# Kernel tuning notes

Measured on AMD Instinct MI355X. Metric: run time of the kernel, lower is better.

Reference implementation:

```python
import jax, jax.numpy as jnp
import numpy as np

HIDDEN_DIM = 2048
NUM_EXPERTS = 64
TOP_K = 8
NUM_TOKENS = 16384


def setup_inputs() -> dict:
    key = jax.random.key(0)
    k_x, k_w, k_b = jax.random.split(key, 3)
    X = jax.random.normal(k_x, (NUM_TOKENS, HIDDEN_DIM), dtype=jnp.float32)
    # nn.Linear(hidden_dim, num_experts): weight [out, in], bias [out]
    bound = 1.0 / np.sqrt(HIDDEN_DIM)
    W_gate = jax.random.uniform(k_w, (NUM_EXPERTS, HIDDEN_DIM), jnp.float32, -bound, bound)
    b_gate = jax.random.uniform(k_b, (NUM_EXPERTS,), jnp.float32, -bound, bound)
    return {"X": X, "W_gate": W_gate, "b_gate": b_gate}


def reference(X, W_gate, b_gate):
    # gate linear: [T, H] @ [H, E] + [E] -> [T, E]
    router_logits = jnp.einsum('th,eh->te', X, W_gate) + b_gate
    # softmax in float32 (matches dtype=torch.float)
    router_probs = jax.nn.softmax(router_logits.astype(jnp.float32), axis=-1)
    # top-k over experts: [T, K]
    router_weights, selected_experts_indices = jax.lax.top_k(router_probs, TOP_K)
    router_weights = router_weights / jnp.sum(router_weights, axis=-1, keepdims=True)
    router_weights = router_weights.astype(X.dtype)
    # one-hot [T, K, E] -> permute(2,1,0) -> [E, K, T]
    expert_mask = jax.nn.one_hot(selected_experts_indices, NUM_EXPERTS, dtype=jnp.int64 if jax.config.jax_enable_x64 else jnp.int32)
    expert_mask = jnp.transpose(expert_mask, (2, 1, 0))
    return (router_logits, router_weights, selected_experts_indices.astype(jnp.int32), expert_mask)
```

## Files before the change

### kernel.cpp

```cpp
#include <hip/hip_runtime.h>

#define NT 16384
#define NH 2048
#define NE 64
#define TOPK 8

#define TB 32
#define KSTEPS 64
#define KQ 4
#define KSW (KSTEPS / KQ)

#define LOFF 0
#define WOFF (NT * NE)
#define IOFF (WOFF + NT * TOPK)
#define MOFF (IOFF + NT * TOPK)

typedef __attribute__((ext_vector_type(8))) short short8;
typedef __attribute__((ext_vector_type(4))) float floatx4;

union FragU { uint4 u; short8 s; };

__device__ __forceinline__ unsigned pack3(float a, float b, unsigned& w1, unsigned& w2) {
    unsigned au = __float_as_uint(a), bu = __float_as_uint(b);
    unsigned ah0 = au & 0xFFFF0000u, bh0 = bu & 0xFFFF0000u;
    float ra = a - __uint_as_float(ah0);
    float rb = b - __uint_as_float(bh0);
    unsigned ar = __float_as_uint(ra), br = __float_as_uint(rb);
    unsigned ah1 = ar & 0xFFFF0000u, bh1 = br & 0xFFFF0000u;
    float sa = ra - __uint_as_float(ah1);
    float sb = rb - __uint_as_float(bh1);
    w1 = bh1 | (ah1 >> 16);
    w2 = (__float_as_uint(sb) & 0xFFFF0000u) | (__float_as_uint(sa) >> 16);
    return bh0 | (ah0 >> 16);
}

__global__ __launch_bounds__(64)
void wconv_kernel(const float* __restrict__ Wg, uint4* __restrict__ wsp) {
    const int b = blockIdx.x;
    const int t = b >> 2, g = b & 3;
    const int l = threadIdx.x;
    const int e  = g * 16 + (l & 15);
    const int k0 = t * 32 + (l >> 4) * 8;
    const float* src = Wg + (size_t)e * NH + k0;
    float4 w0 = *(const float4*)src;
    float4 w1 = *(const float4*)(src + 4);
    unsigned u1[4], u2[4];
    uint4 p0;
    p0.x = pack3(w0.x, w0.y, u1[0], u2[0]);
    p0.y = pack3(w0.z, w0.w, u1[1], u2[1]);
    p0.z = pack3(w1.x, w1.y, u1[2], u2[2]);
    p0.w = pack3(w1.z, w1.w, u1[3], u2[3]);
    uint4* dst = wsp + (size_t)((t * 4 + g) * 3) * 64 + l;
    dst[0]   = p0;
    dst[64]  = make_uint4(u1[0], u1[1], u1[2], u1[3]);
    dst[128] = make_uint4(u2[0], u2[1], u2[2], u2[3]);
}

__global__ __launch_bounds__(512, 4)
void router_kernel(const float* __restrict__ X, const uint4* __restrict__ wsp,
                   const float* __restrict__ bg, float* __restrict__ out) {
    __shared__ __align__(16) float P[KQ][TB][68];
    __shared__ __align__(16) float Ls[TB][68];

    const int tid = threadIdx.x;
    const int w   = tid >> 6;
    const int kh  = w & 3;
    const int th  = w >> 2;
    const int l   = tid & 63;
    const int lr  = l & 15, lq = l >> 4;
    const int tbase = blockIdx.x * TB;

    floatx4 acc[4];
#pragma unroll
    for (int g = 0; g < 4; g++) acc[g] = (floatx4)0.0f;

    const float* xp0 = X + (size_t)(tbase + th * 16 + lr) * NH + kh * (KSW * 32) + lq * 8;
    const uint4* wp = wsp + (size_t)(kh * KSW) * 12 * 64 + l;

    float4 a0lo = *(const float4*)xp0;
    float4 a0hi = *(const float4*)(xp0 + 4);

    {
        float4 z = make_float4(0.f, 0.f, 0.f, 0.f);
#pragma unroll
        for (int m = 0; m < 8; m++) {
            int f2  = tid + 512 * m;
            int seg = f2 >> 3;
            int off = (f2 & 7) << 2;
            *(float4*)(out + MOFF + (size_t)seg * NT + tbase + off) = z;
        }
    }

#pragma unroll 2
    for (int t = 0; t < KSW; t++) {
        FragU b[4][3];
        const uint4* wt = wp + t * 768;
#pragma unroll
        for (int g = 0; g < 4; g++)
#pragma unroll
            for (int p = 0; p < 3; p++)
                b[g][p].u = wt[(g * 3 + p) * 64];

        FragU af[3];
        {
            unsigned u1[4], u2[4];
            uint4 q;
            q.x = pack3(a0lo.x, a0lo.y, u1[0], u2[0]);
            q.y = pack3(a0lo.z, a0lo.w, u1[1], u2[1]);
            q.z = pack3(a0hi.x, a0hi.y, u1[2], u2[2]);
            q.w = pack3(a0hi.z, a0hi.w, u1[3], u2[3]);
            af[0].u = q;
            af[1].u = make_uint4(u1[0], u1[1], u1[2], u1[3]);
            af[2].u = make_uint4(u2[0], u2[1], u2[2], u2[3]);
        }

        if (t + 1 < KSW) {
            const float* nx0 = xp0 + (t + 1) * 32;
            a0lo = *(const float4*)nx0;
            a0hi = *(const float4*)(nx0 + 4);
        }

        __builtin_amdgcn_s_setprio(1);
#pragma unroll
        for (int g = 0; g < 4; g++) {
            acc[g] = __builtin_amdgcn_mfma_f32_16x16x32_bf16(af[0].s, b[g][0].s, acc[g], 0, 0, 0);
            acc[g] = __builtin_amdgcn_mfma_f32_16x16x32_bf16(af[0].s, b[g][1].s, acc[g], 0, 0, 0);
            acc[g] = __builtin_amdgcn_mfma_f32_16x16x32_bf16(af[1].s, b[g][0].s, acc[g], 0, 0, 0);
            acc[g] = __builtin_amdgcn_mfma_f32_16x16x32_bf16(af[1].s, b[g][1].s, acc[g], 0, 0, 0);
            acc[g] = __builtin_amdgcn_mfma_f32_16x16x32_bf16(af[0].s, b[g][2].s, acc[g], 0, 0, 0);
            acc[g] = __builtin_amdgcn_mfma_f32_16x16x32_bf16(af[2].s, b[g][0].s, acc[g], 0, 0, 0);
        }
        __builtin_amdgcn_s_setprio(0);
    }

#pragma unroll
    for (int g = 0; g < 4; g++)
#pragma unroll
        for (int r = 0; r < 4; r++)
            P[kh][th * 16 + lq * 4 + r][g * 16 + lr] = acc[g][r];
    __syncthreads();

    {
        int f4  = tid;
        int tok = f4 >> 4;
        int e4  = (f4 & 15) << 2;
        float4 s0 = *(float4*)&P[0][tok][e4];
        float4 s1 = *(float4*)&P[1][tok][e4];
        float4 s2 = *(float4*)&P[2][tok][e4];
        float4 s3 = *(float4*)&P[3][tok][e4];
        float4 bb = *(const float4*)(bg + e4);
        float4 v;
        v.x = s0.x + s1.x + s2.x + s3.x + bb.x;
        v.y = s0.y + s1.y + s2.y + s3.y + bb.y;
        v.z = s0.z + s1.z + s2.z + s3.z + bb.z;
        v.w = s0.w + s1.w + s2.w + s3.w + bb.w;
        *(float4*)&Ls[tok][e4] = v;
        *(float4*)(out + LOFF + (size_t)tbase * NE + (size_t)f4 * 4) = v;
    }
    __syncthreads();

    if (tid < 256) {
        const int tok = tid >> 3;
        const int el  = tid & 7;
        float4 va = *(float4*)&Ls[tok][el * 8];
        float4 vb = *(float4*)&Ls[tok][el * 8 + 4];
        float v[8] = {va.x, va.y, va.z, va.w, vb.x, vb.y, vb.z, vb.w};

        unsigned msk = 0;
        float m0 = 0.f, ssum = 0.f, myv = 0.f;
        int myi = 0;
#pragma unroll
        for (int r = 0; r < 8; r++) {
            float bv = -3.0e38f; int bi = 64;
#pragma unroll
            for (int j = 0; j < 8; j++) {
                bool better = (((msk >> j) & 1u) == 0u) && (v[j] > bv);
                bv = better ? v[j] : bv;
                bi = better ? (el * 8 + j) : bi;
            }
#pragma unroll
            for (int s2 = 1; s2 < 8; s2 <<= 1) {
                float ov = __shfl_xor(bv, s2);
                int   oi = __shfl_xor(bi, s2);
                bool take = (ov > bv) || (ov == bv && oi < bi);
                bv = take ? ov : bv;
                bi = take ? oi : bi;
            }
            if ((bi >> 3) == el) msk |= (1u << (bi & 7));
            if (r == 0) m0 = bv;
            ssum += __expf(bv - m0);
            if (r == el) { myv = bv; myi = bi; }
        }
        float wgt = __expf(myv - m0) / ssum;
        size_t gt = (size_t)(tbase + tok);
        out[WOFF + gt * TOPK + el] = wgt;
        out[IOFF + gt * TOPK + el] = (float)myi;
        out[MOFF + (size_t)myi * (TOPK * NT) + (size_t)el * NT + gt] = 1.0f;
    }
}

extern "C" void kernel_launch(void* const* d_in, const int* in_sizes, int n_in,
                              void* d_out, int out_size, void* d_ws, size_t ws_size,
                              hipStream_t stream) {
    const float* X  = (const float*)d_in[0];
    const float* Wg = (const float*)d_in[1];
    const float* bg = (const float*)d_in[2];
    float* out = (float*)d_out;
    uint4* wsp = (uint4*)d_ws;

    hipLaunchKernelGGL(wconv_kernel, dim3(KSTEPS * 4), dim3(64), 0, stream, Wg, wsp);
    hipLaunchKernelGGL(router_kernel, dim3(NT / TB), dim3(512), 0, stream,
                       X, (const uint4*)wsp, bg, out);
}
```

Baseline: 241.4 us.

## Restage X through LDS with 32x32 MFMA and split top-k into separate kernel

The GEMM now loads X tiles into LDS asynchronously with global_load_lds and double buffering, using an XOR swizzle, and switches from 16x16x32 to 32x32x16 bf16 MFMA with a new weight packing layout. Zeroing of the expert mask moves into the prep kernel. The top-k/softmax stage moves into a third kernel that rereads logits from global memory. The aim is better X load coalescing and MFMA efficiency, at the cost of an extra launch, an extra logits round trip and a per-step barrier.

Result: faster. 224.0 us (-7.2%).

```diff
diff --git a/kernel.cpp b/kernel.cpp
--- a/kernel.cpp
+++ b/kernel.cpp
@@ -6,9 +6,7 @@
 #define TOPK 8
 
 #define TB 32
-#define KSTEPS 64
-#define KQ 4
-#define KSW (KSTEPS / KQ)
+#define NSS 16
 
 #define LOFF 0
 #define WOFF (NT * NE)
@@ -16,9 +14,15 @@
 #define MOFF (IOFF + NT * TOPK)
 
 typedef __attribute__((ext_vector_type(8))) short short8;
-typedef __attribute__((ext_vector_type(4))) float floatx4;
+typedef __attribute__((ext_vector_type(16))) float floatx16;
 
 union FragU { uint4 u; short8 s; };
+
+__device__ __forceinline__ void glds16(const void* g, void* l) {
+    __builtin_amdgcn_global_load_lds(
+        (const __attribute__((address_space(1))) unsigned int*)g,
+        (__attribute__((address_space(3))) unsigned int*)l, 16, 0, 0);
+}
 
 __device__ __forceinline__ unsigned pack3(float a, float b, unsigned& w1, unsigned& w2) {
     unsigned au = __float_as_uint(a), bu = __float_as_uint(b);
@@ -34,169 +38,181 @@
     return bh0 | (ah0 >> 16);
 }
 
-__global__ __launch_bounds__(64)
-void wconv_kernel(const float* __restrict__ Wg, uint4* __restrict__ wsp) {
+__global__ __launch_bounds__(256)
+void prep_kernel(const float* __restrict__ Wg, uint4* __restrict__ wsp,
+                 float* __restrict__ out) {
     const int b = blockIdx.x;
-    const int t = b >> 2, g = b & 3;
-    const int l = threadIdx.x;
-    const int e  = g * 16 + (l & 15);
-    const int k0 = t * 32 + (l >> 4) * 8;
-    const float* src = Wg + (size_t)e * NH + k0;
-    float4 w0 = *(const float4*)src;
-    float4 w1 = *(const float4*)(src + 4);
-    unsigned u1[4], u2[4];
-    uint4 p0;
-    p0.x = pack3(w0.x, w0.y, u1[0], u2[0]);
-    p0.y = pack3(w0.z, w0.w, u1[1], u2[1]);
-    p0.z = pack3(w1.x, w1.y, u1[2], u2[2]);
-    p0.w = pack3(w1.z, w1.w, u1[3], u2[3]);
-    uint4* dst = wsp + (size_t)((t * 4 + g) * 3) * 64 + l;
-    dst[0]   = p0;
-    dst[64]  = make_uint4(u1[0], u1[1], u1[2], u1[3]);
-    dst[128] = make_uint4(u2[0], u2[1], u2[2], u2[3]);
+    const int tid = threadIdx.x;
+
+    float4 z = make_float4(0.f, 0.f, 0.f, 0.f);
+    float4* mp = (float4*)(out + MOFF) + (size_t)b * 8192 + tid;
+#pragma unroll
+    for (int it = 0; it < 32; it++) mp[it * 256] = z;
+
+    if (tid < 64) {
+        const int t = b >> 2, g = (b >> 1) & 1, h = b & 1;
+        const int l = tid;
+        const int e  = g * 32 + (l & 31);
+        const int k0 = t * 32 + h * 16 + (l >> 5) * 8;
+        const float* src = Wg + (size_t)e * NH + k0;
+        float4 w0 = *(const float4*)src;
+        float4 w1 = *(const float4*)(src + 4);
+        unsigned u1[4], u2[4];
+        uint4 p0;
+        p0.x = pack3(w0.x, w0.y, u1[0], u2[0]);
+        p0.y = pack3(w0.z, w0.w, u1[1], u2[1]);
+        p0.z = pack3(w1.x, w1.y, u1[2], u2[2]);
+        p0.w = pack3(w1.z, w1.w, u1[3], u2[3]);
+        const size_t idx0 = (size_t)((t * 2 + g) * 3) * 2 + h;
+        uint4* dst = wsp + idx0 * 64 + l;
+        dst[0]   = p0;
+        dst[128] = make_uint4(u1[0], u1[1], u1[2], u1[3]);
+        dst[256] = make_uint4(u2[0], u2[1], u2[2], u2[3]);
+    }
 }
 
 __global__ __launch_bounds__(512, 4)
-void router_kernel(const float* __restrict__ X, const uint4* __restrict__ wsp,
-                   const float* __restrict__ bg, float* __restrict__ out) {
-    __shared__ __align__(16) float P[KQ][TB][68];
-    __shared__ __align__(16) float Ls[TB][68];
+void gemm_kernel(const float* __restrict__ X, const uint4* __restrict__ wsp,
+                 const float* __restrict__ bg, float* __restrict__ out) {
+    __shared__ float XS[2][4][32][32];
+    __shared__ float P[4][TB][68];
 
     const int tid = threadIdx.x;
-    const int w   = tid >> 6;
-    const int kh  = w & 3;
-    const int th  = w >> 2;
+    const int wv  = tid >> 6;
     const int l   = tid & 63;
-    const int lr  = l & 15, lq = l >> 4;
+    const int eh  = wv & 1;
+    const int kq  = wv >> 1;
+    const int l31 = l & 31;
+    const int lh  = l >> 5;
     const int tbase = blockIdx.x * TB;
 
-    floatx4 acc[4];
-#pragma unroll
-    for (int g = 0; g < 4; g++) acc[g] = (floatx4)0.0f;
-
-    const float* xp0 = X + (size_t)(tbase + th * 16 + lr) * NH + kh * (KSW * 32) + lq * 8;
-    const uint4* wp = wsp + (size_t)(kh * KSW) * 12 * 64 + l;
-
-    float4 a0lo = *(const float4*)xp0;
-    float4 a0hi = *(const float4*)(xp0 + 4);
+    floatx16 acc = (floatx16)0.0f;
+
+    const int j0 = wv * 2, j1 = wv * 2 + 1;
+    const int q0 = j0 >> 2, r80 = (j0 & 3) * 8;
+    const int q1 = j1 >> 2, r81 = (j1 & 3) * 8;
+    const float* src0 = X + (size_t)(tbase + r80 + (l >> 3)) * NH + q0 * 512
+                          + (((l & 7) ^ ((l >> 3) & 7)) << 2);
+    const float* src1 = X + (size_t)(tbase + r81 + (l >> 3)) * NH + q1 * 512
+                          + (((l & 7) ^ ((l >> 3) & 7)) << 2);
+
+#define STAGE(ss_, s_) do { \
+    glds16(src0 + (ss_) * 32, &XS[s_][q0][r80][0]); \
+    glds16(src1 + (ss_) * 32, &XS[s_][q1][r81][0]); \
+} while (0)
+
+    STAGE(0, 0);
+    __syncthreads();
+
+#pragma unroll 2
+    for (int t = 0; t < NSS; t++) {
+        const int slot = t & 1;
+        const int T = kq * NSS + t;
+        const uint4* bt = wsp + (size_t)((T * 2 + eh) * 6) * 64 + l;
+
+        if (t + 1 < NSS) STAGE(t + 1, slot ^ 1);
+
+        const float* xr = &XS[slot][kq][l31][0];
+        const int s7 = l & 7;
+        const int gb = lh * 2;
+
+#pragma unroll
+        for (int h = 0; h < 2; h++) {
+            FragU b0, b1, b2;
+            b0.u = bt[(0 * 2 + h) * 64];
+            b1.u = bt[(1 * 2 + h) * 64];
+            b2.u = bt[(2 * 2 + h) * 64];
+
+            float4 r0 = *(const float4*)(xr + (((gb + 4 * h) ^ s7) << 2));
+            float4 r1 = *(const float4*)(xr + (((gb + 4 * h + 1) ^ s7) << 2));
+
+            FragU a0, a1, a2;
+            {
+                unsigned u1[4], u2[4];
+                uint4 q;
+                q.x = pack3(r0.x, r0.y, u1[0], u2[0]);
+                q.y = pack3(r0.z, r0.w, u1[1], u2[1]);
+                q.z = pack3(r1.x, r1.y, u1[2], u2[2]);
+                q.w = pack3(r1.z, r1.w, u1[3], u2[3]);
+                a0.u = q;
+                a1.u = make_uint4(u1[0], u1[1], u1[2], u1[3]);
+                a2.u = make_uint4(u2[0], u2[1], u2[2], u2[3]);
+            }
+
+            __builtin_amdgcn_s_setprio(1);
+            acc = __builtin_amdgcn_mfma_f32_32x32x16_bf16(a0.s, b0.s, acc, 0, 0, 0);
+            acc = __builtin_amdgcn_mfma_f32_32x32x16_bf16(a0.s, b1.s, acc, 0, 0, 0);
+            acc = __builtin_amdgcn_mfma_f32_32x32x16_bf16(a1.s, b0.s, acc, 0, 0, 0);
+            acc = __builtin_amdgcn_mfma_f32_32x32x16_bf16(a1.s, b1.s, acc, 0, 0, 0);
+            acc = __builtin_amdgcn_mfma_f32_32x32x16_bf16(a0.s, b2.s, acc, 0, 0, 0);
+            acc = __builtin_amdgcn_mfma_f32_32x32x16_bf16(a2.s, b0.s, acc, 0, 0, 0);
+            __builtin_amdgcn_s_setprio(0);
+        }
+        __syncthreads();
+    }
+
+#pragma unroll
+    for (int r = 0; r < 16; r++)
+        P[kq][(r & 3) + 8 * (r >> 2) + 4 * lh][eh * 32 + l31] = acc[r];
+    __syncthreads();
 
     {
-        float4 z = make_float4(0.f, 0.f, 0.f, 0.f);
-#pragma unroll
-        for (int m = 0; m < 8; m++) {
-            int f2  = tid + 512 * m;
-            int seg = f2 >> 3;
-            int off = (f2 & 7) << 2;
-            *(float4*)(out + MOFF + (size_t)seg * NT + tbase + off) = z;
-        }
-    }
-
-#pragma unroll 2
-    for (int t = 0; t < KSW; t++) {
-        FragU b[4][3];
-        const uint4* wt = wp + t * 768;
-#pragma unroll
-        for (int g = 0; g < 4; g++)
-#pragma unroll
-            for (int p = 0; p < 3; p++)
-                b[g][p].u = wt[(g * 3 + p) * 64];
-
-        FragU af[3];
-        {
-            unsigned u1[4], u2[4];
-            uint4 q;
-            q.x = pack3(a0lo.x, a0lo.y, u1[0], u2[0]);
-            q.y = pack3(a0lo.z, a0lo.w, u1[1], u2[1]);
-            q.z = pack3(a0hi.x, a0hi.y, u1[2], u2[2]);
-            q.w = pack3(a0hi.z, a0hi.w, u1[3], u2[3]);
-            af[0].u = q;
-            af[1].u = make_uint4(u1[0], u1[1], u1[2], u1[3]);
-            af[2].u = make_uint4(u2[0], u2[1], u2[2], u2[3]);
-        }
-
-        if (t + 1 < KSW) {
-            const float* nx0 = xp0 + (t + 1) * 32;
-            a0lo = *(const float4*)nx0;
-            a0hi = *(const float4*)(nx0 + 4);
-        }
-
-        __builtin_amdgcn_s_setprio(1);
-#pragma unroll
-        for (int g = 0; g < 4; g++) {
-            acc[g] = __builtin_amdgcn_mfma_f32_16x16x32_bf16(af[0].s, b[g][0].s, acc[g], 0, 0, 0);
-            acc[g] = __builtin_amdgcn_mfma_f32_16x16x32_bf16(af[0].s, b[g][1].s, acc[g], 0, 0, 0);
-            acc[g] = __builtin_amdgcn_mfma_f32_16x16x32_bf16(af[1].s, b[g][0].s, acc[g], 0, 0, 0);
-            acc[g] = __builtin_amdgcn_mfma_f32_16x16x32_bf16(af[1].s, b[g][1].s, acc[g], 0, 0, 0);
-            acc[g] = __builtin_amdgcn_mfma_f32_16x16x32_bf16(af[0].s, b[g][2].s, acc[g], 0, 0, 0);
-            acc[g] = __builtin_amdgcn_mfma_f32_16x16x32_bf16(af[2].s, b[g][0].s, acc[g], 0, 0, 0);
-        }
-        __builtin_amdgcn_s_setprio(0);
-    }
-
-#pragma unroll
-    for (int g = 0; g < 4; g++)
-#pragma unroll
-        for (int r = 0; r < 4; r++)
-            P[kh][th * 16 + lq * 4 + r][g * 16 + lr] = acc[g][r];
-    __syncthreads();
-
-    {
-        int f4  = tid;
-        int tok = f4 >> 4;
-        int e4  = (f4 & 15) << 2;
-        float4 s0 = *(float4*)&P[0][tok][e4];
-        float4 s1 = *(float4*)&P[1][tok][e4];
-        float4 s2 = *(float4*)&P[2][tok][e4];
-        float4 s3 = *(float4*)&P[3][tok][e4];
+        const int tok = tid >> 4;
+        const int e4  = (tid & 15) << 2;
+        float4 s0 = *(const float4*)&P[0][tok][e4];
+        float4 s1 = *(const float4*)&P[1][tok][e4];
+        float4 s2 = *(const float4*)&P[2][tok][e4];
+        float4 s3 = *(const float4*)&P[3][tok][e4];
         float4 bb = *(const float4*)(bg + e4);
         float4 v;
         v.x = s0.x + s1.x + s2.x + s3.x + bb.x;
         v.y = s0.y + s1.y + s2.y + s3.y + bb.y;
         v.z = s0.z + s1.z + s2.z + s3.z + bb.z;
         v.w = s0.w + s1.w + s2.w + s3.w + bb.w;
-        *(float4*)&Ls[tok][e4] = v;
-        *(float4*)(out + LOFF + (size_t)tbase * NE + (size_t)f4 * 4) = v;
-    }
-    __syncthreads();
-
-    if (tid < 256) {
-        const int tok = tid >> 3;
-        const int el  = tid & 7;
-        float4 va = *(float4*)&Ls[tok][el * 8];
-        float4 vb = *(float4*)&Ls[tok][el * 8 + 4];
-        float v[8] = {va.x, va.y, va.z, va.w, vb.x, vb.y, vb.z, vb.w};
-
-        unsigned msk = 0;
-        float m0 = 0.f, ssum = 0.f, myv = 0.f;
-        int myi = 0;
-#pragma unroll
-        for (int r = 0; r < 8; r++) {
-            float bv = -3.0e38f; int bi = 64;
-#pragma unroll
-            for (int j = 0; j < 8; j++) {
-                bool better = (((msk >> j) & 1u) == 0u) && (v[j] > bv);
-                bv = better ? v[j] : bv;
-                bi = better ? (el * 8 + j) : bi;
-            }
-#pragma unroll
-            for (int s2 = 1; s2 < 8; s2 <<= 1) {
-                float ov = __shfl_xor(bv, s2);
-                int   oi = __shfl_xor(bi, s2);
-                bool take = (ov > bv) || (ov == bv && oi < bi);
-                bv = take ? ov : bv;
-                bi = take ? oi : bi;
-            }
-            if ((bi >> 3) == el) msk |= (1u << (bi & 7));
-            if (r == 0) m0 = bv;
-            ssum += __expf(bv - m0);
-            if (r == el) { myv = bv; myi = bi; }
+        *(float4*)(out + LOFF + (size_t)(tbase + tok) * NE + e4) = v;
+    }
+}
+
+__global__ __launch_bounds__(512)
+void topk_kernel(const float* __restrict__ out_logits, float* __restrict__ out) {
+    const int tid = threadIdx.x;
+    const int tok = blockIdx.x * 64 + (tid >> 3);
+    const int el  = tid & 7;
+    const float* lrow = out_logits + (size_t)tok * NE + el * 8;
+    float4 va = *(const float4*)lrow;
+    float4 vb = *(const float4*)(lrow + 4);
+    float v[8] = {va.x, va.y, va.z, va.w, vb.x, vb.y, vb.z, vb.w};
+
+    unsigned msk = 0;
+    float m0 = 0.f, ssum = 0.f, myv = 0.f;
+    int myi = 0;
+#pragma unroll
+    for (int r = 0; r < 8; r++) {
+        float bv = -3.0e38f; int bi = 64;
+#pragma unroll
+        for (int j = 0; j < 8; j++) {
+            bool better = (((msk >> j) & 1u) == 0u) && (v[j] > bv);
+            bv = better ? v[j] : bv;
+            bi = better ? (el * 8 + j) : bi;
         }
-        float wgt = __expf(myv - m0) / ssum;
-        size_t gt = (size_t)(tbase + tok);
-        out[WOFF + gt * TOPK + el] = wgt;
-        out[IOFF + gt * TOPK + el] = (float)myi;
-        out[MOFF + (size_t)myi * (TOPK * NT) + (size_t)el * NT + gt] = 1.0f;
-    }
+#pragma unroll
+        for (int s2 = 1; s2 < 8; s2 <<= 1) {
+            float ov = __shfl_xor(bv, s2);
+            int   oi = __shfl_xor(bi, s2);
+            bool take = (ov > bv) || (ov == bv && oi < bi);
+            bv = take ? ov : bv;
+            bi = take ? oi : bi;
+        }
+        if ((bi >> 3) == el) msk |= (1u << (bi & 7));
+        if (r == 0) m0 = bv;
+        ssum += __expf(bv - m0);
+        if (r == el) { myv = bv; myi = bi; }
+    }
+    float wgt = __expf(myv - m0) / ssum;
+    size_t gt = (size_t)tok;
+    out[WOFF + gt * TOPK + el] = wgt;
+    out[IOFF + gt * TOPK + el] = (float)myi;
+    out[MOFF + (size_t)myi * (TOPK * NT) + (size_t)el * NT + gt] = 1.0f;
 }
 
 extern "C" void kernel_launch(void* const* d_in, const int* in_sizes, int n_in,
@@ -208,7 +224,9 @@
     float* out = (float*)d_out;
     uint4* wsp = (uint4*)d_ws;
 
-    hipLaunchKernelGGL(wconv_kernel, dim3(KSTEPS * 4), dim3(64), 0, stream, Wg, wsp);
-    hipLaunchKernelGGL(router_kernel, dim3(NT / TB), dim3(512), 0, stream,
+    hipLaunchKernelGGL(prep_kernel, dim3(256), dim3(256), 0, stream, Wg, wsp, out);
+    hipLaunchKernelGGL(gemm_kernel, dim3(NT / TB), dim3(512), 0, stream,
                        X, (const uint4*)wsp, bg, out);
-}
+    hipLaunchKernelGGL(topk_kernel, dim3(NT / 64), dim3(512), 0, stream,
+                       out + LOFF, out);
+}
```
